# Optimization experiments

Measured on AMD Instinct MI355X. Metric: run time of the kernel, lower is better.

## Reference

```python
import jax, jax.numpy as jnp
import numpy as np

B, N, D = 4096, 64, 512
LN_EPS = 1e-5


def setup_inputs() -> dict:
    key = jax.random.key(0)
    k1, k2 = jax.random.split(key)
    return {
        "embeddings": jax.random.normal(k1, (B, N, D), dtype=jnp.float32),
        "ln_gamma": jnp.ones((D,), dtype=jnp.float32),
        "ln_beta": jnp.zeros((D,), dtype=jnp.float32),
        "Wv": jax.random.normal(k2, (D, 1), dtype=jnp.float32) * (1.0 / np.sqrt(D)),
        "bv": jnp.zeros((1,), dtype=jnp.float32),
    }


def reference(embeddings, ln_gamma, ln_beta, Wv, bv):
    # LayerNorm over last dim
    mu = jnp.mean(embeddings, axis=-1, keepdims=True)
    var = jnp.mean(jnp.square(embeddings - mu), axis=-1, keepdims=True)
    e = (embeddings - mu) * jax.lax.rsqrt(var + LN_EPS) * ln_gamma + ln_beta

    query = e[:, :1, :]          # [B, 1, D]
    key_v = e[:, 1:, :]          # [B, N-1, D] (key == value)

    qk = jnp.tanh(query * key_v)                 # broadcasted elementwise mul + tanh
    scores = (qk @ Wv + bv)[..., 0]              # [B, N-1] tiny D->1 projection
    alphas = jax.nn.softmax(scores, axis=-1)[..., None]  # [B, N-1, 1]

    em_a = alphas * key_v                        # softmax-weighted values
    return jnp.concatenate([query, em_a], axis=-2)  # [B, N, D]
```

## Files before the change

### kernel.cpp

```cpp
#include <hip/hip_runtime.h>
#include <math.h>

#define NROWS 64
#define DCOLS 512
#define HCOL  256
#define BDIM  512
#define RPW   8
#define BPB   8

typedef float f32x4 __attribute__((ext_vector_type(4)));

__device__ __forceinline__ void wave_reduce_sum2(float& a, float& b) {
#pragma unroll
    for (int off = 32; off > 0; off >>= 1) {
        a += __shfl_xor(a, off, 64);
        b += __shfl_xor(b, off, 64);
    }
}
__device__ __forceinline__ float wave_reduce_sum(float v) {
#pragma unroll
    for (int off = 32; off > 0; off >>= 1)
        v += __shfl_xor(v, off, 64);
    return v;
}

__device__ __forceinline__ float hsum8(f32x4 a, f32x4 b) {
    return ((a.x + a.y) + (a.z + a.w)) + ((b.x + b.y) + (b.z + b.w));
}
__device__ __forceinline__ float hsumsq8(f32x4 a, f32x4 b) {
    return (a.x*a.x + a.y*a.y + a.z*a.z + a.w*a.w)
         + (b.x*b.x + b.y*b.y + b.z*b.z + b.w*b.w);
}

__device__ __forceinline__ float fast_tanh(float x) {
    float e = __expf(2.0f * x);
    return 1.0f - 2.0f / (e + 1.0f);
}

__device__ __forceinline__ void lds_barrier() {
    asm volatile("s_waitcnt lgkmcnt(0)" ::: "memory");
    __builtin_amdgcn_s_barrier();
}

__global__ __launch_bounds__(BDIM, 4) void fused_ln_attn_kernel(
    const float* __restrict__ emb,
    const float* __restrict__ gamma,
    const float* __restrict__ beta,
    const float* __restrict__ Wv,
    const float* __restrict__ bv,
    float* __restrict__ out,
    int B)
{
    __shared__ __align__(16) float s_e1[NROWS * HCOL];
    __shared__ __align__(16) float s_q[DCOLS];
    __shared__ __align__(16) float s_g[DCOLS];
    __shared__ __align__(16) float s_b[DCOLS];
    __shared__ __align__(16) float s_w[DCOLS];
    __shared__ float s_den[RPW];

    const int tid  = threadIdx.x;
    const int wave = tid >> 6;
    const int lane = tid & 63;
    const int c0   = lane << 2;
    const int c1   = HCOL + c0;
    const int r0   = wave * RPW;

    s_g[tid] = gamma[tid];
    s_b[tid] = beta[tid];
    s_w[tid] = Wv[tid];
    const float bias = bv[0];

    const int bstart = blockIdx.x * BPB;

    f32x4 cx0[RPW];
    {
        const float* eb = emb + (size_t)bstart * (NROWS * DCOLS);
#pragma unroll
        for (int i = 0; i < RPW; ++i)
            cx0[i] = *(const f32x4*)(eb + (r0 + i) * DCOLS + c0);
    }
    lds_barrier();

#pragma unroll 1
    for (int t = 0; t < BPB; ++t) {
        const int bb = bstart + t;
        if (bb >= B) break;
        const float* eb = emb + (size_t)bb * (NROWS * DCOLS);
        float*       ob = out + (size_t)bb * (NROWS * DCOLS);

        f32x4 e0[RPW];
        {
            const f32x4 g0 = *(const f32x4*)(s_g + c0);
            const f32x4 g1 = *(const f32x4*)(s_g + c1);
            const f32x4 b0 = *(const f32x4*)(s_b + c0);
            const f32x4 b1 = *(const f32x4*)(s_b + c1);
#pragma unroll
            for (int i = 0; i < RPW; ++i) {
                const int r = r0 + i;
                const f32x4 x0 = cx0[i];
                const f32x4 x1 = *(const f32x4*)(eb + r * DCOLS + c1);

                float s = hsum8(x0, x1), ss = hsumsq8(x0, x1);
                wave_reduce_sum2(s, ss);

                const float mu  = s * (1.0f / (float)DCOLS);
                const float var = ss * (1.0f / (float)DCOLS) - mu * mu;
                const float rs  = rsqrtf(var + 1e-5f);

                e0[i] = (x0 - mu) * rs * g0 + b0;
                const f32x4 t1 = (x1 - mu) * rs * g1 + b1;
                *(f32x4*)(s_e1 + r * HCOL + c0) = t1;

                if (wave == 0 && i == 0) {
                    *(f32x4*)(s_q + c0) = e0[0];
                    *(f32x4*)(s_q + c1) = t1;
                    __builtin_nontemporal_store(e0[0], (f32x4*)(ob + c0));
                    __builtin_nontemporal_store(t1,    (f32x4*)(ob + c1));
                }
            }
        }

        if (t + 1 < BPB) {
            const float* nb = eb + NROWS * DCOLS;
#pragma unroll
            for (int i = 0; i < RPW; ++i)
                cx0[i] = *(const f32x4*)(nb + (r0 + i) * DCOLS + c0);
        }
        __builtin_amdgcn_sched_barrier(0);

        lds_barrier();

        const f32x4 q0 = *(const f32x4*)(s_q + c0);
        const f32x4 q1 = *(const f32x4*)(s_q + c1);
        const f32x4 w0 = *(const f32x4*)(s_w + c0);
        const f32x4 w1 = *(const f32x4*)(s_w + c1);

        float ex[RPW];
        float denw = 0.0f;
#pragma unroll
        for (int i = 0; i < RPW; ++i) {
            const int r = r0 + i;
            const f32x4 t1 = *(const f32x4*)(s_e1 + r * HCOL + c0);
            float p;
            p  = fast_tanh(q0.x * e0[i].x) * w0.x;
            p += fast_tanh(q0.y * e0[i].y) * w0.y;
            p += fast_tanh(q0.z * e0[i].z) * w0.z;
            p += fast_tanh(q0.w * e0[i].w) * w0.w;
            p += fast_tanh(q1.x * t1.x) * w1.x;
            p += fast_tanh(q1.y * t1.y) * w1.y;
            p += fast_tanh(q1.z * t1.z) * w1.z;
            p += fast_tanh(q1.w * t1.w) * w1.w;
            const float tot = wave_reduce_sum(p) + bias;
            const float e   = __expf(tot);
            ex[i] = (r == 0) ? 0.0f : e;
            denw += ex[i];
        }
        if (lane == 0) s_den[wave] = denw;

        lds_barrier();

        float den = 0.0f;
#pragma unroll
        for (int w = 0; w < RPW; ++w) den += s_den[w];
        const float inv = 1.0f / den;

#pragma unroll
        for (int i = 0; i < RPW; ++i) {
            const int r = r0 + i;
            if (r == 0) continue;
            const float a  = ex[i] * inv;
            const f32x4 t1 = *(const f32x4*)(s_e1 + r * HCOL + c0);
            __builtin_nontemporal_store(e0[i] * a, (f32x4*)(ob + r * DCOLS + c0));
            __builtin_nontemporal_store(t1 * a,    (f32x4*)(ob + r * DCOLS + c1));
        }
    }
}

extern "C" void kernel_launch(void* const* d_in, const int* in_sizes, int n_in,
                              void* d_out, int out_size, void* d_ws, size_t ws_size,
                              hipStream_t stream) {
    const float* emb   = (const float*)d_in[0];
    const float* gamma = (const float*)d_in[1];
    const float* beta  = (const float*)d_in[2];
    const float* Wv    = (const float*)d_in[3];
    const float* bv    = (const float*)d_in[4];
    float* out = (float*)d_out;

    const int B = in_sizes[0] / (NROWS * DCOLS);
    const int grid = (B + BPB - 1) / BPB;
    fused_ln_attn_kernel<<<grid, BDIM, 0, stream>>>(emb, gamma, beta, Wv, bv, out, B);
}
```

Baseline: 221.9 us.

## Prefetch second half-row via global_load_lds and recompute query per wave

The second half of each row is now loaded straight into LDS with global_load_lds, issued right after the previous batch's output for that row is written, so it overlaps with the store phase. Every wave recomputes the LayerNorm of the query row from prefetched registers, which removes the s_q LDS exchange and one block barrier per batch. The softmax denominator array is double-buffered so the removed barrier does not cause a race. In exchange there is a full vmcnt(0) wait at the top of each iteration, redundant query-row normalization in every wave, and ordering risk because each row's LDS slot is reused across batches.

```diff
diff --git a/kernel.cpp b/kernel.cpp
--- a/kernel.cpp
+++ b/kernel.cpp
@@ -1,5 +1,6 @@
 #include <hip/hip_runtime.h>
 #include <math.h>
+#include <stdint.h>
 
 #define NROWS 64
 #define DCOLS 512
@@ -40,6 +41,13 @@
 __device__ __forceinline__ void lds_barrier() {
     asm volatile("s_waitcnt lgkmcnt(0)" ::: "memory");
     __builtin_amdgcn_s_barrier();
+}
+
+__device__ __forceinline__ void glds16(const float* g, float* l) {
+    __builtin_amdgcn_global_load_lds(
+        (const __attribute__((address_space(1))) void*)g,
+        (__attribute__((address_space(3)))       void*)l,
+        16, 0, 0);
 }
 
 __global__ __launch_bounds__(BDIM, 4) void fused_ln_attn_kernel(
@@ -51,12 +59,11 @@
     float* __restrict__ out,
     int B)
 {
-    __shared__ __align__(16) float s_e1[NROWS * HCOL];
-    __shared__ __align__(16) float s_q[DCOLS];
+    __shared__ __align__(16) float s_buf[NROWS * HCOL];
     __shared__ __align__(16) float s_g[DCOLS];
     __shared__ __align__(16) float s_b[DCOLS];
     __shared__ __align__(16) float s_w[DCOLS];
-    __shared__ float s_den[RPW];
+    __shared__ float s_den[2][RPW];
 
     const int tid  = threadIdx.x;
     const int wave = tid >> 6;
@@ -72,12 +79,17 @@
 
     const int bstart = blockIdx.x * BPB;
 
-    f32x4 cx0[RPW];
+    f32x4 cx0[RPW], qxa, qxb;
     {
         const float* eb = emb + (size_t)bstart * (NROWS * DCOLS);
 #pragma unroll
-        for (int i = 0; i < RPW; ++i)
-            cx0[i] = *(const f32x4*)(eb + (r0 + i) * DCOLS + c0);
+        for (int i = 0; i < RPW; ++i) {
+            const int r = r0 + i;
+            glds16(eb + r * DCOLS + c1, s_buf + r * HCOL);
+            cx0[i] = *(const f32x4*)(eb + r * DCOLS + c0);
+        }
+        qxa = *(const f32x4*)(eb + c0);
+        qxb = *(const f32x4*)(eb + c1);
     }
     lds_barrier();
 
@@ -88,7 +100,11 @@
         const float* eb = emb + (size_t)bb * (NROWS * DCOLS);
         float*       ob = out + (size_t)bb * (NROWS * DCOLS);
 
+        asm volatile("s_waitcnt vmcnt(0)" ::: "memory");
+        __builtin_amdgcn_sched_barrier(0);
+
         f32x4 e0[RPW];
+        f32x4 q0, q1;
         {
             const f32x4 g0 = *(const f32x4*)(s_g + c0);
             const f32x4 g1 = *(const f32x4*)(s_g + c1);
@@ -98,7 +114,7 @@
             for (int i = 0; i < RPW; ++i) {
                 const int r = r0 + i;
                 const f32x4 x0 = cx0[i];
-                const f32x4 x1 = *(const f32x4*)(eb + r * DCOLS + c1);
+                const f32x4 x1 = *(const f32x4*)(s_buf + r * HCOL + c0);
 
                 float s = hsum8(x0, x1), ss = hsumsq8(x0, x1);
                 wave_reduce_sum2(s, ss);
@@ -109,15 +125,21 @@
 
                 e0[i] = (x0 - mu) * rs * g0 + b0;
                 const f32x4 t1 = (x1 - mu) * rs * g1 + b1;
-                *(f32x4*)(s_e1 + r * HCOL + c0) = t1;
+                *(f32x4*)(s_buf + r * HCOL + c0) = t1;
 
                 if (wave == 0 && i == 0) {
-                    *(f32x4*)(s_q + c0) = e0[0];
-                    *(f32x4*)(s_q + c1) = t1;
                     __builtin_nontemporal_store(e0[0], (f32x4*)(ob + c0));
                     __builtin_nontemporal_store(t1,    (f32x4*)(ob + c1));
                 }
             }
+
+            float s = hsum8(qxa, qxb), ss = hsumsq8(qxa, qxb);
+            wave_reduce_sum2(s, ss);
+            const float mu  = s * (1.0f / (float)DCOLS);
+            const float var = ss * (1.0f / (float)DCOLS) - mu * mu;
+            const float rs  = rsqrtf(var + 1e-5f);
+            q0 = (qxa - mu) * rs * g0 + b0;
+            q1 = (qxb - mu) * rs * g1 + b1;
         }
 
         if (t + 1 < BPB) {
@@ -125,22 +147,19 @@
 #pragma unroll
             for (int i = 0; i < RPW; ++i)
                 cx0[i] = *(const f32x4*)(nb + (r0 + i) * DCOLS + c0);
+            qxa = *(const f32x4*)(nb + c0);
+            qxb = *(const f32x4*)(nb + c1);
         }
         __builtin_amdgcn_sched_barrier(0);
 
-        lds_barrier();
-
-        const f32x4 q0 = *(const f32x4*)(s_q + c0);
-        const f32x4 q1 = *(const f32x4*)(s_q + c1);
         const f32x4 w0 = *(const f32x4*)(s_w + c0);
         const f32x4 w1 = *(const f32x4*)(s_w + c1);
-
         float ex[RPW];
         float denw = 0.0f;
 #pragma unroll
         for (int i = 0; i < RPW; ++i) {
             const int r = r0 + i;
-            const f32x4 t1 = *(const f32x4*)(s_e1 + r * HCOL + c0);
+            const f32x4 t1 = *(const f32x4*)(s_buf + r * HCOL + c0);
             float p;
             p  = fast_tanh(q0.x * e0[i].x) * w0.x;
             p += fast_tanh(q0.y * e0[i].y) * w0.y;
@@ -155,23 +174,27 @@
             ex[i] = (r == 0) ? 0.0f : e;
             denw += ex[i];
         }
-        if (lane == 0) s_den[wave] = denw;
+        if (lane == 0) s_den[t & 1][wave] = denw;
 
         lds_barrier();
 
         float den = 0.0f;
 #pragma unroll
-        for (int w = 0; w < RPW; ++w) den += s_den[w];
+        for (int w = 0; w < RPW; ++w) den += s_den[t & 1][w];
         const float inv = 1.0f / den;
 
 #pragma unroll
         for (int i = 0; i < RPW; ++i) {
             const int r = r0 + i;
-            if (r == 0) continue;
-            const float a  = ex[i] * inv;
-            const f32x4 t1 = *(const f32x4*)(s_e1 + r * HCOL + c0);
-            __builtin_nontemporal_store(e0[i] * a, (f32x4*)(ob + r * DCOLS + c0));
-            __builtin_nontemporal_store(t1 * a,    (f32x4*)(ob + r * DCOLS + c1));
+            if (r > 0) {
+                const float a  = ex[i] * inv;
+                const f32x4 t1 = *(const f32x4*)(s_buf + r * HCOL + c0);
+                __builtin_nontemporal_store(e0[i] * a, (f32x4*)(ob + r * DCOLS + c0));
+                __builtin_nontemporal_store(t1 * a,    (f32x4*)(ob + r * DCOLS + c1));
+            }
+            if (t + 1 < BPB) {
+                glds16(eb + NROWS * DCOLS + r * DCOLS + c1, s_buf + r * HCOL);
+            }
         }
     }
 }
```

After: 297.7 us. 34.2% more time.

## Store half-row LayerNorm output as bf16 in LDS and launch one block per batch

Applied to the files above, without the earlier changes.

Stores the second half of each normalized row and the projection weights in shared memory as bf16 instead of fp32, halving LDS use to allow more resident blocks. Drops the persistent multi-batch loop with register prefetch and launches one block per batch element. The output for the second half of each row is reconstructed from bf16, which adds rounding error to the result, and the cross-batch load prefetch is lost.

```diff
diff --git a/kernel.cpp b/kernel.cpp
--- a/kernel.cpp
+++ b/kernel.cpp
@@ -5,10 +5,11 @@
 #define DCOLS 512
 #define HCOL  256
 #define BDIM  512
+#define NWV   8
 #define RPW   8
-#define BPB   8
 
 typedef float f32x4 __attribute__((ext_vector_type(4)));
+typedef unsigned short u16x4 __attribute__((ext_vector_type(4)));
 
 __device__ __forceinline__ void wave_reduce_sum2(float& a, float& b) {
 #pragma unroll
@@ -37,6 +38,16 @@
     return 1.0f - 2.0f / (e + 1.0f);
 }
 
+__device__ __forceinline__ unsigned short f2b(float f) {
+    union { float f; unsigned int u; } v; v.f = f;
+    unsigned int r = (v.u + 0x7FFFu + ((v.u >> 16) & 1u)) >> 16;
+    return (unsigned short)r;
+}
+__device__ __forceinline__ float b2f(unsigned short h) {
+    union { unsigned int u; float f; } v; v.u = ((unsigned int)h) << 16;
+    return v.f;
+}
+
 __device__ __forceinline__ void lds_barrier() {
     asm volatile("s_waitcnt lgkmcnt(0)" ::: "memory");
     __builtin_amdgcn_s_barrier();
@@ -48,15 +59,14 @@
     const float* __restrict__ beta,
     const float* __restrict__ Wv,
     const float* __restrict__ bv,
-    float* __restrict__ out,
-    int B)
+    float* __restrict__ out)
 {
-    __shared__ __align__(16) float s_e1[NROWS * HCOL];
+    __shared__ unsigned short      s_e1[NROWS * HCOL];
     __shared__ __align__(16) float s_q[DCOLS];
     __shared__ __align__(16) float s_g[DCOLS];
     __shared__ __align__(16) float s_b[DCOLS];
-    __shared__ __align__(16) float s_w[DCOLS];
-    __shared__ float s_den[RPW];
+    __shared__ unsigned short      s_w[DCOLS];
+    __shared__ float s_den[NWV];
 
     const int tid  = threadIdx.x;
     const int wave = tid >> 6;
@@ -67,112 +77,103 @@
 
     s_g[tid] = gamma[tid];
     s_b[tid] = beta[tid];
-    s_w[tid] = Wv[tid];
+    s_w[tid] = f2b(Wv[tid]);
     const float bias = bv[0];
 
-    const int bstart = blockIdx.x * BPB;
+    const size_t base = (size_t)blockIdx.x * (size_t)(NROWS * DCOLS);
+    const float* eb = emb + base;
+    float*       ob = out + base;
 
-    f32x4 cx0[RPW];
-    {
-        const float* eb = emb + (size_t)bstart * (NROWS * DCOLS);
-#pragma unroll
-        for (int i = 0; i < RPW; ++i)
-            cx0[i] = *(const f32x4*)(eb + (r0 + i) * DCOLS + c0);
-    }
     lds_barrier();
 
-#pragma unroll 1
-    for (int t = 0; t < BPB; ++t) {
-        const int bb = bstart + t;
-        if (bb >= B) break;
-        const float* eb = emb + (size_t)bb * (NROWS * DCOLS);
-        float*       ob = out + (size_t)bb * (NROWS * DCOLS);
-
-        f32x4 e0[RPW];
-        {
-            const f32x4 g0 = *(const f32x4*)(s_g + c0);
-            const f32x4 g1 = *(const f32x4*)(s_g + c1);
-            const f32x4 b0 = *(const f32x4*)(s_b + c0);
-            const f32x4 b1 = *(const f32x4*)(s_b + c1);
-#pragma unroll
-            for (int i = 0; i < RPW; ++i) {
-                const int r = r0 + i;
-                const f32x4 x0 = cx0[i];
-                const f32x4 x1 = *(const f32x4*)(eb + r * DCOLS + c1);
-
-                float s = hsum8(x0, x1), ss = hsumsq8(x0, x1);
-                wave_reduce_sum2(s, ss);
-
-                const float mu  = s * (1.0f / (float)DCOLS);
-                const float var = ss * (1.0f / (float)DCOLS) - mu * mu;
-                const float rs  = rsqrtf(var + 1e-5f);
-
-                e0[i] = (x0 - mu) * rs * g0 + b0;
-                const f32x4 t1 = (x1 - mu) * rs * g1 + b1;
-                *(f32x4*)(s_e1 + r * HCOL + c0) = t1;
-
-                if (wave == 0 && i == 0) {
-                    *(f32x4*)(s_q + c0) = e0[0];
-                    *(f32x4*)(s_q + c1) = t1;
-                    __builtin_nontemporal_store(e0[0], (f32x4*)(ob + c0));
-                    __builtin_nontemporal_store(t1,    (f32x4*)(ob + c1));
-                }
-            }
-        }
-
-        if (t + 1 < BPB) {
-            const float* nb = eb + NROWS * DCOLS;
-#pragma unroll
-            for (int i = 0; i < RPW; ++i)
-                cx0[i] = *(const f32x4*)(nb + (r0 + i) * DCOLS + c0);
-        }
-        __builtin_amdgcn_sched_barrier(0);
-
-        lds_barrier();
-
-        const f32x4 q0 = *(const f32x4*)(s_q + c0);
-        const f32x4 q1 = *(const f32x4*)(s_q + c1);
-        const f32x4 w0 = *(const f32x4*)(s_w + c0);
-        const f32x4 w1 = *(const f32x4*)(s_w + c1);
-
-        float ex[RPW];
-        float denw = 0.0f;
+    f32x4 e0[RPW];
+    {
+        const f32x4 g0 = *(const f32x4*)(s_g + c0);
+        const f32x4 g1 = *(const f32x4*)(s_g + c1);
+        const f32x4 b0 = *(const f32x4*)(s_b + c0);
+        const f32x4 b1 = *(const f32x4*)(s_b + c1);
 #pragma unroll
         for (int i = 0; i < RPW; ++i) {
             const int r = r0 + i;
-            const f32x4 t1 = *(const f32x4*)(s_e1 + r * HCOL + c0);
-            float p;
-            p  = fast_tanh(q0.x * e0[i].x) * w0.x;
-            p += fast_tanh(q0.y * e0[i].y) * w0.y;
-            p += fast_tanh(q0.z * e0[i].z) * w0.z;
-            p += fast_tanh(q0.w * e0[i].w) * w0.w;
-            p += fast_tanh(q1.x * t1.x) * w1.x;
-            p += fast_tanh(q1.y * t1.y) * w1.y;
-            p += fast_tanh(q1.z * t1.z) * w1.z;
-            p += fast_tanh(q1.w * t1.w) * w1.w;
-            const float tot = wave_reduce_sum(p) + bias;
-            const float e   = __expf(tot);
-            ex[i] = (r == 0) ? 0.0f : e;
-            denw += ex[i];
+            const f32x4 x0 = *(const f32x4*)(eb + r * DCOLS + c0);
+            const f32x4 x1 = *(const f32x4*)(eb + r * DCOLS + c1);
+
+            float s = hsum8(x0, x1), ss = hsumsq8(x0, x1);
+            wave_reduce_sum2(s, ss);
+
+            const float mu  = s * (1.0f / (float)DCOLS);
+            const float var = ss * (1.0f / (float)DCOLS) - mu * mu;
+            const float rs  = rsqrtf(var + 1e-5f);
+
+            e0[i] = (x0 - mu) * rs * g0 + b0;
+            const f32x4 t1 = (x1 - mu) * rs * g1 + b1;
+
+            u16x4 p;
+            p.x = f2b(t1.x); p.y = f2b(t1.y); p.z = f2b(t1.z); p.w = f2b(t1.w);
+            *(u16x4*)(s_e1 + r * HCOL + c0) = p;
+
+            if (wave == 0 && i == 0) {
+                *(f32x4*)(s_q + c0) = e0[0];
+                *(f32x4*)(s_q + c1) = t1;
+                __builtin_nontemporal_store(e0[0], (f32x4*)(ob + c0));
+                __builtin_nontemporal_store(t1,    (f32x4*)(ob + c1));
+            }
         }
-        if (lane == 0) s_den[wave] = denw;
+    }
 
-        lds_barrier();
+    lds_barrier();
 
-        float den = 0.0f;
+    const f32x4 q0 = *(const f32x4*)(s_q + c0);
+    const f32x4 q1 = *(const f32x4*)(s_q + c1);
+    f32x4 w0, w1;
+    {
+        const u16x4 wa = *(const u16x4*)(s_w + c0);
+        const u16x4 wb = *(const u16x4*)(s_w + c1);
+        w0.x = b2f(wa.x); w0.y = b2f(wa.y); w0.z = b2f(wa.z); w0.w = b2f(wa.w);
+        w1.x = b2f(wb.x); w1.y = b2f(wb.y); w1.z = b2f(wb.z); w1.w = b2f(wb.w);
+    }
+
+    float ex[RPW];
+    float denw = 0.0f;
 #pragma unroll
-        for (int w = 0; w < RPW; ++w) den += s_den[w];
-        const float inv = 1.0f / den;
+    for (int i = 0; i < RPW; ++i) {
+        const int r = r0 + i;
+        const u16x4 pe = *(const u16x4*)(s_e1 + r * HCOL + c0);
+        f32x4 e1;
+        e1.x = b2f(pe.x); e1.y = b2f(pe.y); e1.z = b2f(pe.z); e1.w = b2f(pe.w);
+        float p;
+        p  = fast_tanh(q0.x * e0[i].x) * w0.x;
+        p += fast_tanh(q0.y * e0[i].y) * w0.y;
+        p += fast_tanh(q0.z * e0[i].z) * w0.z;
+        p += fast_tanh(q0.w * e0[i].w) * w0.w;
+        p += fast_tanh(q1.x * e1.x) * w1.x;
+        p += fast_tanh(q1.y * e1.y) * w1.y;
+        p += fast_tanh(q1.z * e1.z) * w1.z;
+        p += fast_tanh(q1.w * e1.w) * w1.w;
+        const float tot = wave_reduce_sum(p) + bias;
+        const float e   = __expf(tot);
+        ex[i] = (r == 0) ? 0.0f : e;
+        denw += ex[i];
+    }
+    if (lane == 0) s_den[wave] = denw;
+
+    lds_barrier();
+
+    float den = 0.0f;
+#pragma unroll
+    for (int w = 0; w < NWV; ++w) den += s_den[w];
+    const float inv = 1.0f / den;
 
 #pragma unroll
-        for (int i = 0; i < RPW; ++i) {
-            const int r = r0 + i;
-            if (r == 0) continue;
-            const float a  = ex[i] * inv;
-            const f32x4 t1 = *(const f32x4*)(s_e1 + r * HCOL + c0);
-            __builtin_nontemporal_store(e0[i] * a, (f32x4*)(ob + r * DCOLS + c0));
-            __builtin_nontemporal_store(t1 * a,    (f32x4*)(ob + r * DCOLS + c1));
-        }
+    for (int i = 0; i < RPW; ++i) {
+        const int r = r0 + i;
+        if (r == 0) continue;
+        const float a = ex[i] * inv;
+        const u16x4 pe = *(const u16x4*)(s_e1 + r * HCOL + c0);
+        f32x4 e1;
+        e1.x = b2f(pe.x); e1.y = b2f(pe.y); e1.z = b2f(pe.z); e1.w = b2f(pe.w);
+        __builtin_nontemporal_store(e0[i] * a, (f32x4*)(ob + r * DCOLS + c0));
+        __builtin_nontemporal_store(e1 * a,    (f32x4*)(ob + r * DCOLS + c1));
     }
 }
 
@@ -187,6 +188,5 @@
     float* out = (float*)d_out;
 
     const int B = in_sizes[0] / (NROWS * DCOLS);
-    const int grid = (B + BPB - 1) / BPB;
-    fused_ln_attn_kernel<<<grid, BDIM, 0, stream>>>(emb, gamma, beta, Wv, bv, out, B);
+    fused_ln_attn_kernel<<<B, BDIM, 0, stream>>>(emb, gamma, beta, Wv, bv, out);
 }
```

Result: no change. 220.0 us (-0.8%).
